# Kernel optimization log

Hardware: AMD Instinct MI355X
Metric: run time of the kernel (lower is better)

The kernel has to match this reference:

```python
import jax, jax.numpy as jnp
import numpy as np

B, T = 64, 4096
ATTN_RNN_DIM, HYPERNET_DIM = 1024, 256
CHANNELS, KERNEL_SIZE, OUT_DIM = 32, 31, 128
PAD = (KERNEL_SIZE - 1) // 2


def setup_inputs() -> dict:
    key = jax.random.key(0)
    ks = jax.random.split(key, 8)
    s = 0.02
    return {
        "query": jax.random.normal(ks[0], (B, ATTN_RNN_DIM), jnp.float32),
        "prev_attn": jax.random.uniform(ks[1], (B, T), jnp.float32),
        "W1": jax.random.normal(ks[2], (HYPERNET_DIM, ATTN_RNN_DIM), jnp.float32) * s,
        "b1": jnp.zeros((HYPERNET_DIM,), jnp.float32),
        "W2": jax.random.normal(ks[3], (CHANNELS * KERNEL_SIZE, HYPERNET_DIM), jnp.float32) * s,
        "b2": jnp.zeros((CHANNELS * KERNEL_SIZE,), jnp.float32),
        "Wfc": jax.random.normal(ks[4], (OUT_DIM, CHANNELS), jnp.float32) * s,
        "bfc": jnp.zeros((OUT_DIM,), jnp.float32),
    }


def reference(query, prev_attn, W1, b1, W2, b2, Wfc, bfc):
    # hypernet: Linear -> tanh -> Linear, producing per-sample conv weights
    h = jnp.tanh(query @ W1.T + b1)                       # [B, hypernet_dim]
    convweight = (h @ W2.T + b2).reshape(B, CHANNELS, KERNEL_SIZE)  # [B, C, K]

    # per-sample depthwise conv1d (cross-correlation, 'same' padding)
    padded = jnp.pad(prev_attn, ((0, 0), (PAD, PAD)))     # [B, T+K-1]
    idx = jnp.arange(KERNEL_SIZE)[:, None] + jnp.arange(T)[None, :]  # [K, T]
    windows = padded[:, idx]                              # [B, K, T]
    x = jnp.einsum('bck,bkt->btc', convweight, windows)   # [B, T, C]

    # output linear
    return x @ Wfc.T + bfc                                # [B, T, out_dim]
```

## Files before the change

kernel.cpp:

```cpp
#include <hip/hip_runtime.h>

#define B 64
#define T 4096
#define AD 1024
#define HD 256
#define CH 32
#define KS 31
#define OD 128
#define PADW 15
#define CWN (CH*KS)
#define TILE_T 64
#define NTILE (T / TILE_T)
#define PADROW 132

__global__ __launch_bounds__(256) void k_hyper1(const float* __restrict__ q,
        const float* __restrict__ W1, const float* __restrict__ b1,
        float* __restrict__ h) {
    int wid  = blockIdx.x * 4 + (threadIdx.x >> 6);
    int lane = threadIdx.x & 63;
    int b = wid >> 8;
    int j = wid & 255;
    const float4* qr = (const float4*)(q  + (size_t)b * AD);
    const float4* wr = (const float4*)(W1 + (size_t)j * AD);
    float s = 0.f;
    #pragma unroll
    for (int m = 0; m < 4; ++m) {
        float4 a = qr[m * 64 + lane];
        float4 w = wr[m * 64 + lane];
        s += a.x * w.x + a.y * w.y + a.z * w.z + a.w * w.w;
    }
    #pragma unroll
    for (int off = 32; off > 0; off >>= 1)
        s += __shfl_down(s, off, 64);
    if (lane == 0) h[b * HD + j] = tanhf(s + b1[j]);
}

__global__ __launch_bounds__(256) void k_cw(const float* __restrict__ h,
        const float* __restrict__ W2, const float* __restrict__ b2,
        float* __restrict__ cw) {
    int b   = blockIdx.x >> 2;
    int qtr = blockIdx.x & 3;
    int tid = threadIdx.x;
    __shared__ float hs[HD];
    hs[tid] = h[(size_t)b * HD + tid];
    __syncthreads();
    int r = qtr * 248 + tid;
    if (tid < 248) {
        const float4* wr = (const float4*)(W2 + (size_t)r * HD);
        float s = 0.f;
        #pragma unroll
        for (int m = 0; m < HD / 4; ++m) {
            float4 w = wr[m];
            s += w.x * hs[4*m+0] + w.y * hs[4*m+1]
               + w.z * hs[4*m+2] + w.w * hs[4*m+3];
        }
        cw[(size_t)b * CWN + r] = s + b2[r];
    }
}

__global__ __launch_bounds__(256) void k_G(const float* __restrict__ cw,
        const float* __restrict__ Wfc, float* __restrict__ Gt) {
    int b   = blockIdx.x >> 2;
    int qtr = blockIdx.x & 3;
    int tid = threadIdx.x;
    __shared__ float cws[CWN];
    __shared__ float wfs_t[CH * OD];
    #pragma unroll
    for (int p = 0; p < 4; ++p) {
        int idx = p * 256 + tid;
        if (idx < CWN) cws[idx] = cw[(size_t)b * CWN + idx];
    }
    #pragma unroll
    for (int p = 0; p < 16; ++p) {
        int idx = p * 256 + tid;
        int o = idx >> 5, c = idx & 31;
        wfs_t[c * OD + o] = Wfc[idx];
    }
    __syncthreads();
    if (tid < 248) {
        int base = qtr * 992 + tid * 4;
        #pragma unroll
        for (int j = 0; j < 4; ++j) {
            int idx = base + j;
            int k = idx >> 7, o = idx & 127;
            float s = 0.f;
            #pragma unroll
            for (int c = 0; c < CH; ++c)
                s += wfs_t[c * OD + o] * cws[c * KS + k];
            Gt[(size_t)b * (KS * OD) + idx] = s;
        }
    }
}

__device__ __forceinline__ void compute_chunk(const float* pa, int s0, float base,
                                              const float (&g)[KS], float (&acc)[8]) {
    float pw[40];
    const float4* lp = (const float4*)(pa + s0);
    #pragma unroll
    for (int q4 = 0; q4 < 10; ++q4) {
        float4 v = lp[q4];
        pw[q4*4+0] = v.x; pw[q4*4+1] = v.y; pw[q4*4+2] = v.z; pw[q4*4+3] = v.w;
    }
    #pragma unroll
    for (int tt = 0; tt < 8; ++tt) {
        float a = base;
        #pragma unroll
        for (int k = 0; k < KS; ++k)
            a += g[k] * pw[tt + k];
        acc[tt] = a;
    }
}

__global__ __launch_bounds__(256, 4) void k_conv(const float* __restrict__ pa_g,
        const float* __restrict__ Gt, const float* __restrict__ bfc,
        float* __restrict__ out) {
    int bid = blockIdx.x;
    int sid = (bid & 7) * 512 + (bid >> 3);
    int b    = sid >> 6;
    int tile = sid & 63;
    int t0   = tile * TILE_T;
    int tid  = threadIdx.x;
    __shared__ float tileo[TILE_T][PADROW];
    __shared__ float pa[TILE_T + 32];

    if (tid < TILE_T + 32) {
        int g = t0 + tid - PADW;
        pa[tid] = (g >= 0 && g < T) ? pa_g[(size_t)b * T + g] : 0.f;
    }
    int o = tid & 127, half = tid >> 7;
    float g[KS];
    #pragma unroll
    for (int k = 0; k < KS; ++k)
        g[k] = Gt[(size_t)b * (KS * OD) + k * OD + o];
    float base = bfc[o];
    __syncthreads();

    #pragma unroll
    for (int c = 0; c < 4; ++c) {
        int s0 = half * 32 + c * 8;
        float acc[8];
        compute_chunk(pa, s0, base, g, acc);
        #pragma unroll
        for (int tt = 0; tt < 8; ++tt)
            tileo[s0 + tt][o] = acc[tt];
    }
    __syncthreads();

    size_t obase = ((size_t)b * T + t0) * OD;
    #pragma unroll
    for (int it = 0; it < 8; ++it) {
        int flat = it * 1024 + tid * 4;
        int t = flat >> 7, oo = flat & 127;
        float4 v = *(const float4*)&tileo[t][oo];
        *(float4*)(out + obase + flat) = v;
    }
}

extern "C" void kernel_launch(void* const* d_in, const int* in_sizes, int n_in,
                              void* d_out, int out_size, void* d_ws, size_t ws_size,
                              hipStream_t stream) {
    const float* query = (const float*)d_in[0];
    const float* prev  = (const float*)d_in[1];
    const float* W1    = (const float*)d_in[2];
    const float* b1    = (const float*)d_in[3];
    const float* W2    = (const float*)d_in[4];
    const float* b2    = (const float*)d_in[5];
    const float* Wfc   = (const float*)d_in[6];
    const float* bfc   = (const float*)d_in[7];
    float* out = (float*)d_out;

    float* h  = (float*)d_ws;
    float* cw = h + B * HD;
    float* Gt = cw + B * CWN;

    k_hyper1<<<dim3(4096), dim3(256), 0, stream>>>(query, W1, b1, h);
    k_cw    <<<dim3(B * 4), dim3(256), 0, stream>>>(h, W2, b2, cw);
    k_G     <<<dim3(B * 4), dim3(256), 0, stream>>>(cw, Wfc, Gt);
    k_conv  <<<dim3(B * NTILE), dim3(256), 0, stream>>>(prev, Gt, bfc, out);
}
```

Baseline: 56.73 us.

## Fuse hypernet kernels into one per-batch block and halve conv tile size

```diff
diff --git a/kernel.cpp b/kernel.cpp
--- a/kernel.cpp
+++ b/kernel.cpp
@@ -9,79 +9,67 @@
 #define OD 128
 #define PADW 15
 #define CWN (CH*KS)
-#define TILE_T 64
+#define TILE_T 32
 #define NTILE (T / TILE_T)
 #define PADROW 132
 
-__global__ __launch_bounds__(256) void k_hyper1(const float* __restrict__ q,
+__global__ __launch_bounds__(1024) void k_hyper(const float* __restrict__ q,
         const float* __restrict__ W1, const float* __restrict__ b1,
-        float* __restrict__ h) {
-    int wid  = blockIdx.x * 4 + (threadIdx.x >> 6);
-    int lane = threadIdx.x & 63;
-    int b = wid >> 8;
-    int j = wid & 255;
-    const float4* qr = (const float4*)(q  + (size_t)b * AD);
-    const float4* wr = (const float4*)(W1 + (size_t)j * AD);
-    float s = 0.f;
-    #pragma unroll
-    for (int m = 0; m < 4; ++m) {
-        float4 a = qr[m * 64 + lane];
-        float4 w = wr[m * 64 + lane];
-        s += a.x * w.x + a.y * w.y + a.z * w.z + a.w * w.w;
-    }
-    #pragma unroll
-    for (int off = 32; off > 0; off >>= 1)
-        s += __shfl_down(s, off, 64);
-    if (lane == 0) h[b * HD + j] = tanhf(s + b1[j]);
-}
-
-__global__ __launch_bounds__(256) void k_cw(const float* __restrict__ h,
         const float* __restrict__ W2, const float* __restrict__ b2,
-        float* __restrict__ cw) {
-    int b   = blockIdx.x >> 2;
-    int qtr = blockIdx.x & 3;
+        const float* __restrict__ Wfc, float* __restrict__ Gt) {
+    int b = blockIdx.x;
     int tid = threadIdx.x;
+    int lane = tid & 63, wv = tid >> 6;
+    __shared__ float qs[AD];
     __shared__ float hs[HD];
-    hs[tid] = h[(size_t)b * HD + tid];
-    __syncthreads();
-    int r = qtr * 248 + tid;
-    if (tid < 248) {
-        const float4* wr = (const float4*)(W2 + (size_t)r * HD);
-        float s = 0.f;
-        #pragma unroll
-        for (int m = 0; m < HD / 4; ++m) {
-            float4 w = wr[m];
-            s += w.x * hs[4*m+0] + w.y * hs[4*m+1]
-               + w.z * hs[4*m+2] + w.w * hs[4*m+3];
-        }
-        cw[(size_t)b * CWN + r] = s + b2[r];
-    }
-}
-
-__global__ __launch_bounds__(256) void k_G(const float* __restrict__ cw,
-        const float* __restrict__ Wfc, float* __restrict__ Gt) {
-    int b   = blockIdx.x >> 2;
-    int qtr = blockIdx.x & 3;
-    int tid = threadIdx.x;
     __shared__ float cws[CWN];
     __shared__ float wfs_t[CH * OD];
+
+    qs[tid] = q[(size_t)b * AD + tid];
     #pragma unroll
     for (int p = 0; p < 4; ++p) {
-        int idx = p * 256 + tid;
-        if (idx < CWN) cws[idx] = cw[(size_t)b * CWN + idx];
-    }
-    #pragma unroll
-    for (int p = 0; p < 16; ++p) {
-        int idx = p * 256 + tid;
+        int idx = p * 1024 + tid;
         int o = idx >> 5, c = idx & 31;
         wfs_t[c * OD + o] = Wfc[idx];
     }
     __syncthreads();
-    if (tid < 248) {
-        int base = qtr * 992 + tid * 4;
+
+    const float4* qs4 = (const float4*)qs;
+    #pragma unroll
+    for (int i = 0; i < 16; ++i) {
+        int j = wv * 16 + i;
+        const float4* wr = (const float4*)(W1 + (size_t)j * AD);
+        float s = 0.f;
         #pragma unroll
-        for (int j = 0; j < 4; ++j) {
-            int idx = base + j;
+        for (int m = 0; m < 4; ++m) {
+            float4 w  = wr[m * 64 + lane];
+            float4 qv = qs4[m * 64 + lane];
+            s += w.x * qv.x + w.y * qv.y + w.z * qv.z + w.w * qv.w;
+        }
+        #pragma unroll
+        for (int off = 32; off > 0; off >>= 1)
+            s += __shfl_down(s, off, 64);
+        if (lane == 0) hs[j] = tanhf(s + b1[j]);
+    }
+    __syncthreads();
+
+    if (tid < CWN) {
+        const float4* wr  = (const float4*)(W2 + (size_t)tid * HD);
+        const float4* hs4 = (const float4*)hs;
+        float s = 0.f;
+        #pragma unroll
+        for (int m = 0; m < HD / 4; ++m) {
+            float4 w = wr[m], hv = hs4[m];
+            s += w.x * hv.x + w.y * hv.y + w.z * hv.z + w.w * hv.w;
+        }
+        cws[tid] = s + b2[tid];
+    }
+    __syncthreads();
+
+    #pragma unroll
+    for (int p = 0; p < 4; ++p) {
+        int idx = p * 1024 + tid;
+        if (idx < KS * OD) {
             int k = idx >> 7, o = idx & 127;
             float s = 0.f;
             #pragma unroll
@@ -111,21 +99,21 @@
     }
 }
 
-__global__ __launch_bounds__(256, 4) void k_conv(const float* __restrict__ pa_g,
+__global__ __launch_bounds__(256, 8) void k_conv(const float* __restrict__ pa_g,
         const float* __restrict__ Gt, const float* __restrict__ bfc,
         float* __restrict__ out) {
-    int bid = blockIdx.x;
-    int sid = (bid & 7) * 512 + (bid >> 3);
-    int b    = sid >> 6;
-    int tile = sid & 63;
+    int bid  = blockIdx.x;
+    int sid  = (bid & 7) * (B * NTILE / 8) + (bid >> 3);
+    int b    = sid >> 7;
+    int tile = sid & 127;
     int t0   = tile * TILE_T;
     int tid  = threadIdx.x;
     __shared__ float tileo[TILE_T][PADROW];
     __shared__ float pa[TILE_T + 32];
 
-    if (tid < TILE_T + 32) {
-        int g = t0 + tid - PADW;
-        pa[tid] = (g >= 0 && g < T) ? pa_g[(size_t)b * T + g] : 0.f;
+    if (tid < TILE_T + 30) {
+        int gg = t0 + tid - PADW;
+        pa[tid] = (gg >= 0 && gg < T) ? pa_g[(size_t)b * T + gg] : 0.f;
     }
     int o = tid & 127, half = tid >> 7;
     float g[KS];
@@ -136,8 +124,8 @@
     __syncthreads();
 
     #pragma unroll
-    for (int c = 0; c < 4; ++c) {
-        int s0 = half * 32 + c * 8;
+    for (int c = 0; c < 2; ++c) {
+        int s0 = half * 16 + c * 8;
         float acc[8];
         compute_chunk(pa, s0, base, g, acc);
         #pragma unroll
@@ -148,7 +136,7 @@
 
     size_t obase = ((size_t)b * T + t0) * OD;
     #pragma unroll
-    for (int it = 0; it < 8; ++it) {
+    for (int it = 0; it < 4; ++it) {
         int flat = it * 1024 + tid * 4;
         int t = flat >> 7, oo = flat & 127;
         float4 v = *(const float4*)&tileo[t][oo];
@@ -169,12 +157,8 @@
     const float* bfc   = (const float*)d_in[7];
     float* out = (float*)d_out;
 
-    float* h  = (float*)d_ws;
-    float* cw = h + B * HD;
-    float* Gt = cw + B * CWN;
+    float* Gt = (float*)d_ws;
 
-    k_hyper1<<<dim3(4096), dim3(256), 0, stream>>>(query, W1, b1, h);
-    k_cw    <<<dim3(B * 4), dim3(256), 0, stream>>>(h, W2, b2, cw);
-    k_G     <<<dim3(B * 4), dim3(256), 0, stream>>>(cw, Wfc, Gt);
-    k_conv  <<<dim3(B * NTILE), dim3(256), 0, stream>>>(prev, Gt, bfc, out);
+    k_hyper<<<dim3(B), dim3(1024), 0, stream>>>(query, W1, b1, W2, b2, Wfc, Gt);
+    k_conv <<<dim3(B * NTILE), dim3(256), 0, stream>>>(prev, Gt, bfc, out);
 }
```

Result: slower. 84.08 us (+48.2%).
